# Optimization experiments

Measured on AMD Instinct MI355X. Metric: run time of the kernel, lower is better.

The kernel has to match this reference:

```python
import jax, jax.numpy as jnp
import numpy as np
from jax import lax

DILATION = 4
H = 512


def prelu(x, alpha):
    # Keras PReLU: max(x,0) + alpha * min(x,0); alpha broadcast over batch dim
    return jnp.maximum(x, 0) + alpha * jnp.minimum(x, 0)


def setup_inputs() -> dict:
    key = jax.random.key(0)
    ks = jax.random.split(key, 7)
    B_, T, Bc = 8, 4096, 128
    x = jax.random.normal(ks[0], (B_, T, Bc), jnp.float32)
    w_bottleneck = jax.random.normal(ks[1], (Bc, H), jnp.float32) * (1.0 / np.sqrt(Bc))
    alpha1 = jax.random.uniform(ks[2], (T, H), jnp.float32) * 0.25
    w_depth = jax.random.normal(ks[3], (3, 1, H), jnp.float32) * (1.0 / np.sqrt(3))
    alpha2 = jax.random.uniform(ks[4], (T, H), jnp.float32) * 0.25
    w_res = jax.random.normal(ks[5], (H, Bc), jnp.float32) * (1.0 / np.sqrt(H))
    w_skip = jax.random.normal(ks[6], (H, 128), jnp.float32) * (1.0 / np.sqrt(H))
    return {"x": x, "w_bottleneck": w_bottleneck, "alpha1": alpha1,
            "w_depth": w_depth, "alpha2": alpha2, "w_res": w_res, "w_skip": w_skip}


def reference(x, w_bottleneck, alpha1, w_depth, alpha2, w_res, w_skip):
    # bottleneck 1x1 conv: (B,T,Bc) @ (Bc,H) -> (B,T,H)
    h = jnp.einsum('btc,ch->bth', x, w_bottleneck)
    h = prelu(h, alpha1)
    # depthwise conv over time, dilation=DILATION, padding SAME, groups=H
    y = lax.conv_general_dilated(
        h, w_depth,
        window_strides=(1,), padding='SAME',
        rhs_dilation=(DILATION,),
        dimension_numbers=('NWC', 'WIO', 'NWC'),
        feature_group_count=H)
    y = prelu(y, alpha2)
    residual = jnp.einsum('bth,hc->btc', y, w_res) + x
    skip = jnp.einsum('bth,hs->bts', y, w_skip)
    return (residual, skip)
```

## Files before the change

### kernel.cpp

```cpp
#include <hip/hip_runtime.h>
#include <hip/hip_bf16.h>

#define NB 8
#define NT 4096
#define NC 128
#define NH 512
#define TB 32

typedef __attribute__((ext_vector_type(8))) short bf16x8;
typedef __attribute__((ext_vector_type(4))) float f32x4;
typedef __attribute__((ext_vector_type(16))) float f32x16;

__device__ __forceinline__ ushort f2bf(float f) {
    uint u = __float_as_uint(f);
    uint r = u + 0x7FFFu + ((u >> 16) & 1u);
    return (ushort)(r >> 16);
}
__device__ __forceinline__ float bf2f(short b) {
    return __uint_as_float(((uint)(ushort)b) << 16);
}
__device__ __forceinline__ int rowof(int reg, int hi) {
    return (reg & 3) + 8 * (reg >> 2) + 4 * hi;
}
__device__ __forceinline__ int swz(int s) {
    return s ^ (((s >> 7) & 3) << 4);
}

#define NWBT 65536
#define NWCT 131072

__global__ __launch_bounds__(512) void prep_weights(
    const float* __restrict__ wb, const float* __restrict__ wres,
    const float* __restrict__ wskip, short* __restrict__ wbt32,
    short* __restrict__ wct)
{
    int i = blockIdx.x * 512 + threadIdx.x;
    if (i < NWBT) {
        int ii = i & 7, l = (i >> 3) & 63, jt = (i >> 9) & 15, kt = i >> 13;
        int k = kt * 16 + (l >> 5) * 8 + ii;
        int j = jt * 32 + (l & 31);
        wbt32[i] = (short)f2bf(wb[(size_t)k * NH + j]);
    } else {
        int i2 = i - NWBT;
        int ii = i2 & 7, l = (i2 >> 3) & 63, jt = (i2 >> 9) & 15, kt = i2 >> 13;
        int k = kt * 32 + (l >> 4) * 8 + ii;
        int j = jt * 16 + (l & 15);
        float v = (j < 128) ? wres[k * NC + j] : wskip[k * NC + (j - 128)];
        wct[i2] = (short)f2bf(v);
    }
}

__global__ __launch_bounds__(512, 4) void conv1d_block_mfma(
    const float* __restrict__ x,
    const float* __restrict__ a1,
    const float* __restrict__ wd,
    const float* __restrict__ a2,
    const short* __restrict__ wbt32,
    const short* __restrict__ wct,
    float* __restrict__ out)
{
    __shared__ short xs[1024 * 8];
    __shared__ short ys[16384];

    const int tid  = threadIdx.x;
    const int lane = tid & 63;
    const int wave = tid >> 6;
    const int b    = blockIdx.x >> 7;
    const int t0   = (blockIdx.x & 127) * TB;
    const int hi   = lane >> 5;
    const int jl   = lane & 15;
    const int rb   = (lane >> 4) * 4;

    #pragma unroll
    for (int it = 0; it < 2; ++it) {
        int chunk = tid + it * 512;
        int mt = chunk >> 9;
        int kt = (chunk >> 6) & 7;
        int l  = chunk & 63;
        int t  = t0 - 4 + mt * 32 + (l & 31);
        int c0 = kt * 16 + (l >> 5) * 8;
        float4 p0 = make_float4(0.f, 0.f, 0.f, 0.f), p1 = p0;
        if (t >= 0 && t < NT) {
            const float* src = &x[((size_t)b * NT + t) * NC + c0];
            p0 = *reinterpret_cast<const float4*>(src);
            p1 = *reinterpret_cast<const float4*>(src + 4);
        }
        bf16x8 s;
        s[0] = (short)f2bf(p0.x); s[1] = (short)f2bf(p0.y);
        s[2] = (short)f2bf(p0.z); s[3] = (short)f2bf(p0.w);
        s[4] = (short)f2bf(p1.x); s[5] = (short)f2bf(p1.y);
        s[6] = (short)f2bf(p1.z); s[7] = (short)f2bf(p1.w);
        *reinterpret_cast<bf16x8*>(&xs[chunk * 8]) = s;
    }
    __syncthreads();

    f32x16 acc1[2][2];
    #pragma unroll
    for (int mt = 0; mt < 2; ++mt)
        #pragma unroll
        for (int n = 0; n < 2; ++n)
            #pragma unroll
            for (int r = 0; r < 16; ++r) acc1[mt][n][r] = 0.f;

    #pragma unroll
    for (int kt = 0; kt < 8; ++kt) {
        bf16x8 af0 = *reinterpret_cast<const bf16x8*>(&xs[((0 * 8 + kt) * 64 + lane) * 8]);
        bf16x8 af1 = *reinterpret_cast<const bf16x8*>(&xs[((1 * 8 + kt) * 64 + lane) * 8]);
        #pragma unroll
        for (int n = 0; n < 2; ++n) {
            int jt = wave * 2 + n;
            bf16x8 bfr = *reinterpret_cast<const bf16x8*>(&wbt32[((kt * 16 + jt) * 64 + lane) * 8]);
            acc1[0][n] = __builtin_amdgcn_mfma_f32_32x32x16_bf16(af0, bfr, acc1[0][n], 0, 0, 0);
            acc1[1][n] = __builtin_amdgcn_mfma_f32_32x32x16_bf16(af1, bfr, acc1[1][n], 0, 0, 0);
        }
    }

    #pragma unroll
    for (int mt = 0; mt < 2; ++mt) {
        #pragma unroll
        for (int n = 0; n < 2; ++n) {
            int j = (wave * 2 + n) * 32 + (lane & 31);
            #pragma unroll
            for (int reg = 0; reg < 16; ++reg) {
                int t = t0 - 4 + mt * 32 + rowof(reg, hi);
                t = min(max(t, 0), NT - 1);
                float al = a1[(size_t)t * NH + j];
                float v  = acc1[mt][n][reg];
                acc1[mt][n][reg] = fmaxf(v, 0.f) + al * fminf(v, 0.f);
            }
        }
    }

    float kw0[2], kw1[2], kw2[2];
    #pragma unroll
    for (int n = 0; n < 2; ++n) {
        int j = (wave * 2 + n) * 32 + (lane & 31);
        kw0[n] = wd[0 * NH + j];
        kw1[n] = wd[1 * NH + j];
        kw2[n] = wd[2 * NH + j];
    }

    #pragma unroll
    for (int n = 0; n < 2; ++n) {
        const int jt = wave * 2 + n;
        const int j  = jt * 32 + (lane & 31);
        #pragma unroll
        for (int reg = 0; reg < 16; ++reg) {
            float vm  = acc1[0][n][reg];
            float h8  = (reg < 12) ? acc1[0][n][reg + 4] : acc1[1][n][reg - 12];
            float sup = (lane < 32) ? h8 : vm;
            float h4  = __shfl_xor(sup, 32);
            float v = kw0[n] * vm + kw1[n] * h4 + kw2[n] * h8;
            float al = a2[(size_t)(t0 + rowof(reg, hi)) * NH + j];
            v = fmaxf(v, 0.f) + al * fminf(v, 0.f);
            int mt2 = reg >> 3;
            int l2  = ((reg & 3) + 8 * ((reg >> 2) & 1) + 4 * hi) | (((lane >> 3) & 3) << 4);
            ys[swz(((mt2 * 16 + jt) * 64 + l2) * 8 + (lane & 7))] = (short)f2bf(v);
        }
    }
    __syncthreads();

    f32x4 acc2[2][2];
    #pragma unroll
    for (int m = 0; m < 2; ++m)
        #pragma unroll
        for (int n = 0; n < 2; ++n)
            acc2[m][n] = (f32x4){0.f, 0.f, 0.f, 0.f};

    #pragma unroll
    for (int kt = 0; kt < 16; ++kt) {
        bf16x8 A0 = *reinterpret_cast<const bf16x8*>(&ys[swz(((0 * 16 + kt) * 64 + lane) * 8)]);
        bf16x8 A1 = *reinterpret_cast<const bf16x8*>(&ys[swz(((1 * 16 + kt) * 64 + lane) * 8)]);
        #pragma unroll
        for (int n = 0; n < 2; ++n) {
            int jt = wave * 2 + n;
            bf16x8 Bf = *reinterpret_cast<const bf16x8*>(&wct[((kt * 16 + jt) * 64 + lane) * 8]);
            acc2[0][n] = __builtin_amdgcn_mfma_f32_16x16x32_bf16(A0, Bf, acc2[0][n], 0, 0, 0);
            acc2[1][n] = __builtin_amdgcn_mfma_f32_16x16x32_bf16(A1, Bf, acc2[1][n], 0, 0, 0);
        }
    }

    #pragma unroll
    for (int m = 0; m < 2; ++m) {
        #pragma unroll
        for (int n = 0; n < 2; ++n) {
            int j = wave * 32 + n * 16 + jl;
            #pragma unroll
            for (int reg = 0; reg < 4; ++reg) {
                int g = m * 16 + rb + reg;
                size_t t = (size_t)(t0 + g);
                float v = acc2[m][n][reg];
                if (j < 128) {
                    int r4   = g + 4;
                    int ladr = (((r4 >> 5) * 8 + (j >> 4)) * 64
                                + ((r4 & 31) + (((j >> 3) & 1) << 5))) * 8 + (j & 7);
                    float xv = bf2f(xs[ladr]);
                    size_t idx = ((size_t)b * NT + t) * NC + j;
                    out[idx] = v + xv;
                } else {
                    size_t idx = ((size_t)b * NT + t) * NC + (j - 128);
                    out[(size_t)NB * NT * NC + idx] = v;
                }
            }
        }
    }
}

extern "C" void kernel_launch(void* const* d_in, const int* in_sizes, int n_in,
                              void* d_out, int out_size, void* d_ws, size_t ws_size,
                              hipStream_t stream) {
    const float* x  = (const float*)d_in[0];
    const float* wb = (const float*)d_in[1];
    const float* a1 = (const float*)d_in[2];
    const float* wd = (const float*)d_in[3];
    const float* a2 = (const float*)d_in[4];
    const float* wr = (const float*)d_in[5];
    const float* wk = (const float*)d_in[6];
    float* out = (float*)d_out;

    short* wbt32 = (short*)d_ws;
    short* wct   = wbt32 + NWBT;

    prep_weights<<<dim3(384), dim3(512), 0, stream>>>(wb, wr, wk, wbt32, wct);
    conv1d_block_mfma<<<dim3(NB * (NT / TB)), dim3(512), 0, stream>>>(
        x, a1, wd, a2, wbt32, wct, out);
}
```

Baseline: 46.78 us.

## Split fused conv block into two kernels staging activations through global memory

Result: slower. 58.84 us (+25.8%).

```diff
diff --git a/kernel.cpp b/kernel.cpp
--- a/kernel.cpp
+++ b/kernel.cpp
@@ -28,6 +28,7 @@
 
 #define NWBT 65536
 #define NWCT 131072
+#define YTILE 16384
 
 __global__ __launch_bounds__(512) void prep_weights(
     const float* __restrict__ wb, const float* __restrict__ wres,
@@ -50,16 +51,189 @@
     }
 }
 
-__global__ __launch_bounds__(512, 4) void conv1d_block_mfma(
-    const float* __restrict__ x,
-    const float* __restrict__ a1,
-    const float* __restrict__ wd,
-    const float* __restrict__ a2,
-    const short* __restrict__ wbt32,
-    const short* __restrict__ wct,
+__global__ __launch_bounds__(512, 4) void conv1d_part1(
+    const float* __restrict__ x, const float* __restrict__ a1,
+    const float* __restrict__ wd, const float* __restrict__ a2,
+    const short* __restrict__ wbt32, short* __restrict__ yg)
+{
+    __shared__ short xs[8192];
+    __shared__ short ys[16384];
+
+    const int tid  = threadIdx.x;
+    const int lane = tid & 63;
+    const int wave = tid >> 6;
+    const int b    = blockIdx.x >> 7;
+    const int t0   = (blockIdx.x & 127) * TB;
+    const int hi   = lane >> 5;
+
+    #pragma unroll
+    for (int it = 0; it < 2; ++it) {
+        int chunk = tid + it * 512;
+        int mt = chunk >> 9;
+        int kt = (chunk >> 6) & 7;
+        int l  = chunk & 63;
+        int t  = t0 - 4 + mt * 32 + (l & 31);
+        int c0 = kt * 16 + (l >> 5) * 8;
+        float4 p0 = make_float4(0.f, 0.f, 0.f, 0.f), p1 = p0;
+        if (t >= 0 && t < NT) {
+            const float* src = &x[((size_t)b * NT + t) * NC + c0];
+            p0 = *reinterpret_cast<const float4*>(src);
+            p1 = *reinterpret_cast<const float4*>(src + 4);
+        }
+        bf16x8 s;
+        s[0] = (short)f2bf(p0.x); s[1] = (short)f2bf(p0.y);
+        s[2] = (short)f2bf(p0.z); s[3] = (short)f2bf(p0.w);
+        s[4] = (short)f2bf(p1.x); s[5] = (short)f2bf(p1.y);
+        s[6] = (short)f2bf(p1.z); s[7] = (short)f2bf(p1.w);
+        *reinterpret_cast<bf16x8*>(&xs[chunk * 8]) = s;
+    }
+    __syncthreads();
+
+    f32x16 acc1[2][2];
+    #pragma unroll
+    for (int mt = 0; mt < 2; ++mt)
+        #pragma unroll
+        for (int n = 0; n < 2; ++n)
+            #pragma unroll
+            for (int r = 0; r < 16; ++r) acc1[mt][n][r] = 0.f;
+
+    #pragma unroll
+    for (int kt = 0; kt < 8; ++kt) {
+        bf16x8 af0 = *reinterpret_cast<const bf16x8*>(&xs[((0 * 8 + kt) * 64 + lane) * 8]);
+        bf16x8 af1 = *reinterpret_cast<const bf16x8*>(&xs[((1 * 8 + kt) * 64 + lane) * 8]);
+        #pragma unroll
+        for (int n = 0; n < 2; ++n) {
+            int jt = wave * 2 + n;
+            bf16x8 bfr = *reinterpret_cast<const bf16x8*>(&wbt32[((kt * 16 + jt) * 64 + lane) * 8]);
+            acc1[0][n] = __builtin_amdgcn_mfma_f32_32x32x16_bf16(af0, bfr, acc1[0][n], 0, 0, 0);
+            acc1[1][n] = __builtin_amdgcn_mfma_f32_32x32x16_bf16(af1, bfr, acc1[1][n], 0, 0, 0);
+        }
+    }
+
+    #pragma unroll
+    for (int mt = 0; mt < 2; ++mt) {
+        #pragma unroll
+        for (int n = 0; n < 2; ++n) {
+            int j = (wave * 2 + n) * 32 + (lane & 31);
+            #pragma unroll
+            for (int reg = 0; reg < 16; ++reg) {
+                int t = t0 - 4 + mt * 32 + rowof(reg, hi);
+                t = min(max(t, 0), NT - 1);
+                float al = a1[(size_t)t * NH + j];
+                float v  = acc1[mt][n][reg];
+                acc1[mt][n][reg] = fmaxf(v, 0.f) + al * fminf(v, 0.f);
+            }
+        }
+    }
+
+    float kw0[2], kw1[2], kw2[2];
+    #pragma unroll
+    for (int n = 0; n < 2; ++n) {
+        int j = (wave * 2 + n) * 32 + (lane & 31);
+        kw0[n] = wd[0 * NH + j];
+        kw1[n] = wd[1 * NH + j];
+        kw2[n] = wd[2 * NH + j];
+    }
+
+    #pragma unroll
+    for (int n = 0; n < 2; ++n) {
+        const int jt = wave * 2 + n;
+        const int j  = jt * 32 + (lane & 31);
+        #pragma unroll
+        for (int reg = 0; reg < 16; ++reg) {
+            float vm  = acc1[0][n][reg];
+            float h8  = (reg < 12) ? acc1[0][n][reg + 4] : acc1[1][n][reg - 12];
+            float sup = (lane < 32) ? h8 : vm;
+            float h4  = __shfl_xor(sup, 32);
+            float v = kw0[n] * vm + kw1[n] * h4 + kw2[n] * h8;
+            float al = a2[(size_t)(t0 + rowof(reg, hi)) * NH + j];
+            v = fmaxf(v, 0.f) + al * fminf(v, 0.f);
+            int mt2 = reg >> 3;
+            int l2  = ((reg & 3) + 8 * ((reg >> 2) & 1) + 4 * hi) | (((lane >> 3) & 3) << 4);
+            ys[swz(((mt2 * 16 + jt) * 64 + l2) * 8 + (lane & 7))] = (short)f2bf(v);
+        }
+    }
+    __syncthreads();
+
+    #pragma unroll
+    for (int it = 0; it < 4; ++it) {
+        int chunk = tid + it * 512;
+        bf16x8 v = *reinterpret_cast<const bf16x8*>(&ys[swz(chunk * 8)]);
+        *reinterpret_cast<bf16x8*>(&yg[(size_t)blockIdx.x * YTILE + chunk * 8]) = v;
+    }
+}
+
+__global__ __launch_bounds__(512, 6) void conv1d_part2(
+    const float* __restrict__ x, const short* __restrict__ yg,
+    const short* __restrict__ wct, float* __restrict__ out)
+{
+    __shared__ short ys2[16384];
+
+    const int tid  = threadIdx.x;
+    const int lane = tid & 63;
+    const int wave = tid >> 6;
+    const int b    = blockIdx.x >> 7;
+    const int t0   = (blockIdx.x & 127) * TB;
+    const int jl   = lane & 15;
+    const int rb   = (lane >> 4) * 4;
+
+    #pragma unroll
+    for (int it = 0; it < 4; ++it) {
+        int chunk = tid + it * 512;
+        bf16x8 v = *reinterpret_cast<const bf16x8*>(&yg[(size_t)blockIdx.x * YTILE + chunk * 8]);
+        *reinterpret_cast<bf16x8*>(&ys2[chunk * 8]) = v;
+    }
+    __syncthreads();
+
+    f32x4 acc2[2][2];
+    #pragma unroll
+    for (int m = 0; m < 2; ++m)
+        #pragma unroll
+        for (int n = 0; n < 2; ++n)
+            acc2[m][n] = (f32x4){0.f, 0.f, 0.f, 0.f};
+
+    #pragma unroll
+    for (int kt = 0; kt < 16; ++kt) {
+        bf16x8 A0 = *reinterpret_cast<const bf16x8*>(&ys2[((0 * 16 + kt) * 64 + lane) * 8]);
+        bf16x8 A1 = *reinterpret_cast<const bf16x8*>(&ys2[((1 * 16 + kt) * 64 + lane) * 8]);
+        #pragma unroll
+        for (int n = 0; n < 2; ++n) {
+            int jt = wave * 2 + n;
+            bf16x8 Bf = *reinterpret_cast<const bf16x8*>(&wct[((kt * 16 + jt) * 64 + lane) * 8]);
+            acc2[0][n] = __builtin_amdgcn_mfma_f32_16x16x32_bf16(A0, Bf, acc2[0][n], 0, 0, 0);
+            acc2[1][n] = __builtin_amdgcn_mfma_f32_16x16x32_bf16(A1, Bf, acc2[1][n], 0, 0, 0);
+        }
+    }
+
+    #pragma unroll
+    for (int m = 0; m < 2; ++m) {
+        #pragma unroll
+        for (int n = 0; n < 2; ++n) {
+            int j = wave * 32 + n * 16 + jl;
+            #pragma unroll
+            for (int reg = 0; reg < 4; ++reg) {
+                int g = m * 16 + rb + reg;
+                size_t t = (size_t)(t0 + g);
+                float v = acc2[m][n][reg];
+                if (j < 128) {
+                    size_t idx = ((size_t)b * NT + t) * NC + j;
+                    out[idx] = v + x[idx];
+                } else {
+                    size_t idx = ((size_t)b * NT + t) * NC + (j - 128);
+                    out[(size_t)NB * NT * NC + idx] = v;
+                }
+            }
+        }
+    }
+}
+
+__global__ __launch_bounds__(512, 4) void conv1d_block_fused(
+    const float* __restrict__ x, const float* __restrict__ a1,
+    const float* __restrict__ wd, const float* __restrict__ a2,
+    const short* __restrict__ wbt32, const short* __restrict__ wct,
     float* __restrict__ out)
 {
-    __shared__ short xs[1024 * 8];
+    __shared__ short xs[8192];
     __shared__ short ys[16384];
 
     const int tid  = threadIdx.x;
@@ -220,8 +394,18 @@
 
     short* wbt32 = (short*)d_ws;
     short* wct   = wbt32 + NWBT;
+    short* yg    = wct + NWCT;
+    const size_t need_split = (size_t)(NWBT + NWCT) * 2 + (size_t)1024 * YTILE * 2;
 
     prep_weights<<<dim3(384), dim3(512), 0, stream>>>(wb, wr, wk, wbt32, wct);
-    conv1d_block_mfma<<<dim3(NB * (NT / TB)), dim3(512), 0, stream>>>(
-        x, a1, wd, a2, wbt32, wct, out);
-}
+
+    if (ws_size >= need_split) {
+        conv1d_part1<<<dim3(NB * (NT / TB)), dim3(512), 0, stream>>>(
+            x, a1, wd, a2, wbt32, yg);
+        conv1d_part2<<<dim3(NB * (NT / TB)), dim3(512), 0, stream>>>(
+            x, yg, wct, out);
+    } else {
+        conv1d_block_fused<<<dim3(NB * (NT / TB)), dim3(512), 0, stream>>>(
+            x, a1, wd, a2, wbt32, wct, out);
+    }
+}
```

## Use 1024-thread blocks with one output tile per wave

Applied to the files above, without the earlier changes.

After: 62.42 us. 1.33x slower.

```diff
diff --git a/kernel.cpp b/kernel.cpp
--- a/kernel.cpp
+++ b/kernel.cpp
@@ -50,7 +50,7 @@
     }
 }
 
-__global__ __launch_bounds__(512, 4) void conv1d_block_mfma(
+__global__ __launch_bounds__(1024, 8) void conv1d_block_mfma(
     const float* __restrict__ x,
     const float* __restrict__ a1,
     const float* __restrict__ wd,
@@ -59,7 +59,7 @@
     const short* __restrict__ wct,
     float* __restrict__ out)
 {
-    __shared__ short xs[1024 * 8];
+    __shared__ short xs[8192];
     __shared__ short ys[16384];
 
     const int tid  = threadIdx.x;
@@ -71,9 +71,8 @@
     const int jl   = lane & 15;
     const int rb   = (lane >> 4) * 4;
 
-    #pragma unroll
-    for (int it = 0; it < 2; ++it) {
-        int chunk = tid + it * 512;
+    {
+        int chunk = tid;
         int mt = chunk >> 9;
         int kt = (chunk >> 6) & 7;
         int l  = chunk & 63;
@@ -94,102 +93,79 @@
     }
     __syncthreads();
 
-    f32x16 acc1[2][2];
-    #pragma unroll
-    for (int mt = 0; mt < 2; ++mt)
-        #pragma unroll
-        for (int n = 0; n < 2; ++n)
-            #pragma unroll
-            for (int r = 0; r < 16; ++r) acc1[mt][n][r] = 0.f;
+    f32x16 acc1a, acc1b;
+    #pragma unroll
+    for (int r = 0; r < 16; ++r) { acc1a[r] = 0.f; acc1b[r] = 0.f; }
 
     #pragma unroll
     for (int kt = 0; kt < 8; ++kt) {
         bf16x8 af0 = *reinterpret_cast<const bf16x8*>(&xs[((0 * 8 + kt) * 64 + lane) * 8]);
         bf16x8 af1 = *reinterpret_cast<const bf16x8*>(&xs[((1 * 8 + kt) * 64 + lane) * 8]);
-        #pragma unroll
-        for (int n = 0; n < 2; ++n) {
-            int jt = wave * 2 + n;
-            bf16x8 bfr = *reinterpret_cast<const bf16x8*>(&wbt32[((kt * 16 + jt) * 64 + lane) * 8]);
-            acc1[0][n] = __builtin_amdgcn_mfma_f32_32x32x16_bf16(af0, bfr, acc1[0][n], 0, 0, 0);
-            acc1[1][n] = __builtin_amdgcn_mfma_f32_32x32x16_bf16(af1, bfr, acc1[1][n], 0, 0, 0);
-        }
-    }
-
-    #pragma unroll
-    for (int mt = 0; mt < 2; ++mt) {
-        #pragma unroll
-        for (int n = 0; n < 2; ++n) {
-            int j = (wave * 2 + n) * 32 + (lane & 31);
-            #pragma unroll
-            for (int reg = 0; reg < 16; ++reg) {
-                int t = t0 - 4 + mt * 32 + rowof(reg, hi);
-                t = min(max(t, 0), NT - 1);
-                float al = a1[(size_t)t * NH + j];
-                float v  = acc1[mt][n][reg];
-                acc1[mt][n][reg] = fmaxf(v, 0.f) + al * fminf(v, 0.f);
-            }
-        }
-    }
-
-    float kw0[2], kw1[2], kw2[2];
-    #pragma unroll
-    for (int n = 0; n < 2; ++n) {
-        int j = (wave * 2 + n) * 32 + (lane & 31);
-        kw0[n] = wd[0 * NH + j];
-        kw1[n] = wd[1 * NH + j];
-        kw2[n] = wd[2 * NH + j];
-    }
-
-    #pragma unroll
-    for (int n = 0; n < 2; ++n) {
-        const int jt = wave * 2 + n;
-        const int j  = jt * 32 + (lane & 31);
-        #pragma unroll
-        for (int reg = 0; reg < 16; ++reg) {
-            float vm  = acc1[0][n][reg];
-            float h8  = (reg < 12) ? acc1[0][n][reg + 4] : acc1[1][n][reg - 12];
-            float sup = (lane < 32) ? h8 : vm;
-            float h4  = __shfl_xor(sup, 32);
-            float v = kw0[n] * vm + kw1[n] * h4 + kw2[n] * h8;
-            float al = a2[(size_t)(t0 + rowof(reg, hi)) * NH + j];
-            v = fmaxf(v, 0.f) + al * fminf(v, 0.f);
-            int mt2 = reg >> 3;
-            int l2  = ((reg & 3) + 8 * ((reg >> 2) & 1) + 4 * hi) | (((lane >> 3) & 3) << 4);
-            ys[swz(((mt2 * 16 + jt) * 64 + l2) * 8 + (lane & 7))] = (short)f2bf(v);
-        }
+        bf16x8 bfr = *reinterpret_cast<const bf16x8*>(&wbt32[((kt * 16 + wave) * 64 + lane) * 8]);
+        acc1a = __builtin_amdgcn_mfma_f32_32x32x16_bf16(af0, bfr, acc1a, 0, 0, 0);
+        acc1b = __builtin_amdgcn_mfma_f32_32x32x16_bf16(af1, bfr, acc1b, 0, 0, 0);
+    }
+
+    const int jh = wave * 32 + (lane & 31);
+    #pragma unroll
+    for (int reg = 0; reg < 16; ++reg) {
+        int t = t0 - 4 + rowof(reg, hi);
+        t = max(t, 0);
+        float al = a1[(size_t)t * NH + jh];
+        float v  = acc1a[reg];
+        acc1a[reg] = fmaxf(v, 0.f) + al * fminf(v, 0.f);
+    }
+    float halo[4];
+    #pragma unroll
+    for (int r = 0; r < 4; ++r) {
+        int t = t0 + 28 + r + 4 * hi;
+        t = min(t, NT - 1);
+        float al = a1[(size_t)t * NH + jh];
+        float v  = acc1b[r];
+        halo[r] = fmaxf(v, 0.f) + al * fminf(v, 0.f);
+    }
+
+    const float k0 = wd[0 * NH + jh];
+    const float k1 = wd[1 * NH + jh];
+    const float k2 = wd[2 * NH + jh];
+
+    #pragma unroll
+    for (int reg = 0; reg < 16; ++reg) {
+        float vm  = acc1a[reg];
+        float h8  = (reg < 12) ? acc1a[reg + 4] : halo[reg - 12];
+        float sup = (lane < 32) ? h8 : vm;
+        float h4  = __shfl_xor(sup, 32);
+        float v = k0 * vm + k1 * h4 + k2 * h8;
+        float al = a2[(size_t)(t0 + rowof(reg, hi)) * NH + jh];
+        v = fmaxf(v, 0.f) + al * fminf(v, 0.f);
+        int mt2 = reg >> 3;
+        int l2  = ((reg & 3) + 8 * ((reg >> 2) & 1) + 4 * hi) | (((lane >> 3) & 3) << 4);
+        ys[swz(((mt2 * 16 + wave) * 64 + l2) * 8 + (lane & 7))] = (short)f2bf(v);
     }
     __syncthreads();
 
-    f32x4 acc2[2][2];
-    #pragma unroll
-    for (int m = 0; m < 2; ++m)
-        #pragma unroll
-        for (int n = 0; n < 2; ++n)
-            acc2[m][n] = (f32x4){0.f, 0.f, 0.f, 0.f};
+    f32x4 acc2[2];
+    acc2[0] = (f32x4){0.f, 0.f, 0.f, 0.f};
+    acc2[1] = (f32x4){0.f, 0.f, 0.f, 0.f};
 
     #pragma unroll
     for (int kt = 0; kt < 16; ++kt) {
         bf16x8 A0 = *reinterpret_cast<const bf16x8*>(&ys[swz(((0 * 16 + kt) * 64 + lane) * 8)]);
         bf16x8 A1 = *reinterpret_cast<const bf16x8*>(&ys[swz(((1 * 16 + kt) * 64 + lane) * 8)]);
+        bf16x8 Bf = *reinterpret_cast<const bf16x8*>(&wct[((kt * 16 + wave) * 64 + lane) * 8]);
+        acc2[0] = __builtin_amdgcn_mfma_f32_16x16x32_bf16(A0, Bf, acc2[0], 0, 0, 0);
+        acc2[1] = __builtin_amdgcn_mfma_f32_16x16x32_bf16(A1, Bf, acc2[1], 0, 0, 0);
+    }
+
+    {
+        const int j = wave * 16 + jl;
         #pragma unroll
-        for (int n = 0; n < 2; ++n) {
-            int jt = wave * 2 + n;
-            bf16x8 Bf = *reinterpret_cast<const bf16x8*>(&wct[((kt * 16 + jt) * 64 + lane) * 8]);
-            acc2[0][n] = __builtin_amdgcn_mfma_f32_16x16x32_bf16(A0, Bf, acc2[0][n], 0, 0, 0);
-            acc2[1][n] = __builtin_amdgcn_mfma_f32_16x16x32_bf16(A1, Bf, acc2[1][n], 0, 0, 0);
-        }
-    }
-
-    #pragma unroll
-    for (int m = 0; m < 2; ++m) {
-        #pragma unroll
-        for (int n = 0; n < 2; ++n) {
-            int j = wave * 32 + n * 16 + jl;
+        for (int m = 0; m < 2; ++m) {
             #pragma unroll
             for (int reg = 0; reg < 4; ++reg) {
                 int g = m * 16 + rb + reg;
                 size_t t = (size_t)(t0 + g);
-                float v = acc2[m][n][reg];
+                float v = acc2[m][reg];
                 if (j < 128) {
                     int r4   = g + 4;
                     int ladr = (((r4 >> 5) * 8 + (j >> 4)) * 64
@@ -222,6 +198,6 @@
     short* wct   = wbt32 + NWBT;
 
     prep_weights<<<dim3(384), dim3(512), 0, stream>>>(wb, wr, wk, wbt32, wct);
-    conv1d_block_mfma<<<dim3(NB * (NT / TB)), dim3(512), 0, stream>>>(
+    conv1d_block_mfma<<<dim3(NB * (NT / TB)), dim3(1024), 0, stream>>>(
         x, a1, wd, a2, wbt32, wct, out);
 }
```
